# Kernel tuning notes

Hardware: AMD Instinct MI355X
Metric: run time of the kernel (lower is better)

The kernel has to match this reference:

```python
import jax, jax.numpy as jnp
import numpy as np

V, E, H, T = 100000, 128, 256, 7
B, S = 64, 512
START, STOP = 5, 6
H2 = H // 2


def setup_inputs() -> dict:
    key = jax.random.key(0)
    ks = jax.random.split(key, 16)
    rn = lambda k, shape, s=0.1: jax.random.normal(k, shape, jnp.float32) * s
    inp = {}
    inp["sentence"] = jax.random.randint(ks[0], (B, S), 0, V)
    inp["tags"] = jax.random.randint(ks[1], (B, S), 0, 5)
    inp["h0"] = jax.random.normal(ks[2], (2, B, H2), jnp.float32)
    inp["c0"] = jax.random.normal(ks[3], (2, B, H2), jnp.float32)
    inp["embedding"] = rn(ks[4], (V, E), 1.0)
    inp["w_ih_f"] = rn(ks[5], (4 * H2, E)); inp["w_hh_f"] = rn(ks[6], (4 * H2, H2))
    inp["b_ih_f"] = rn(ks[7], (4 * H2,)); inp["b_hh_f"] = rn(ks[8], (4 * H2,))
    inp["w_ih_b"] = rn(ks[9], (4 * H2, E)); inp["w_hh_b"] = rn(ks[10], (4 * H2, H2))
    inp["b_ih_b"] = rn(ks[11], (4 * H2,)); inp["b_hh_b"] = rn(ks[12], (4 * H2,))
    inp["w_out"] = rn(ks[13], (T, H)); inp["b_out"] = rn(ks[14], (T,))
    trans = jax.random.normal(ks[15], (T, T), jnp.float32)
    trans = trans.at[START, :].set(-10000.0).at[:, STOP].set(-10000.0)
    inp["transitions"] = trans
    return inp


def _lstm_dir(x, h0, c0, wih, whh, bih, bhh, reverse):
    # x: [S, B, E]; PyTorch gate order i, f, g, o
    def step(carry, xt):
        h, c = carry
        z = xt @ wih.T + h @ whh.T + bih + bhh  # [B, 4*H2]
        i, f, g, o = jnp.split(z, 4, axis=-1)
        c = jax.nn.sigmoid(f) * c + jax.nn.sigmoid(i) * jnp.tanh(g)
        h = jax.nn.sigmoid(o) * jnp.tanh(c)
        return (h, c), h
    _, hs = jax.lax.scan(step, (h0, c0), x, reverse=reverse)
    return hs  # [S, B, H2]


def reference(sentence, tags, h0, c0, embedding, w_ih_f, w_hh_f, b_ih_f, b_hh_f,
              w_ih_b, w_hh_b, b_ih_b, b_hh_b, w_out, b_out, transitions):
    # Embedding; torch code does .view(S, B, -1) on a [B, S, E] tensor (raw
    # reinterpretation) -- replicate with reshape to match the math exactly.
    embeds = embedding[sentence].reshape(S, B, E)
    hf = _lstm_dir(embeds, h0[0], c0[0], w_ih_f, w_hh_f, b_ih_f, b_hh_f, False)
    hb = _lstm_dir(embeds, h0[1], c0[1], w_ih_b, w_hh_b, b_ih_b, b_hh_b, True)
    feats = jnp.concatenate([hf, hb], axis=-1) @ w_out.T + b_out  # [S, B, T]

    # CRF forward algorithm. Original uses transitions.t(), i.e. step score
    # for prev=i -> next=j is transitions[i, j].
    alpha0 = jnp.full((B, T), -10000.0, jnp.float32).at[:, START].set(0.0)
    def crf_step(alpha, feat):
        # [b, i, j]: alpha[b,i] + transitions[i,j]; LSE over i, add emit[b,j]
        a = jax.nn.logsumexp(alpha[:, :, None] + transitions[None, :, :], axis=1) + feat
        return a, None
    alpha, _ = jax.lax.scan(crf_step, alpha0, feats)
    fwd_score = jax.nn.logsumexp(alpha + transitions[STOP][None, :], axis=1)  # [B]

    # Gold path score: transitions[next, prev] + emit[next], per _score_sentence.
    tags_ext = jnp.concatenate([jnp.full((B, 1), START, tags.dtype), tags], axis=1)
    t_prev, t_next = tags_ext[:, :-1], tags_ext[:, 1:]  # [B, S]
    trans_sc = transitions[t_next, t_prev].sum(axis=1)
    emit_sc = jnp.take_along_axis(jnp.transpose(feats, (1, 0, 2)),
                                  t_next[:, :, None], axis=2)[..., 0].sum(axis=1)
    gold = trans_sc + emit_sc + transitions[STOP, tags_ext[:, -1]]
    return jnp.sum(fwd_score - gold) / B
```

## Files before the change

kernel.cpp:

```cpp
#include <hip/hip_runtime.h>

typedef unsigned int u32;
typedef unsigned short u16;
typedef __attribute__((ext_vector_type(8))) short short8;
typedef __attribute__((ext_vector_type(4))) float f32x4;
typedef __attribute__((ext_vector_type(2))) float f32x2;

#define DEV __device__ __forceinline__
#define LOG2E 1.44269504089f

DEV u16 f2bf(float f) {
    u32 u = __float_as_uint(f);
    return (u16)((u + 0x7FFFu + ((u >> 16) & 1u)) >> 16);
}
DEV float bf2f(u16 h) { return __uint_as_float(((u32)h) << 16); }
DEV float frcp(float x) { return __builtin_amdgcn_rcpf(x); }
DEV float fexp2(float x) {
#if __has_builtin(__builtin_amdgcn_exp2f)
    return __builtin_amdgcn_exp2f(x);
#else
    return exp2f(x);
#endif
}
DEV u32 pack_bf16(float a, float b) {
#if __has_builtin(__builtin_amdgcn_cvt_pk_bf16_f32)
    auto v = __builtin_amdgcn_cvt_pk_bf16_f32(a, b);
    u32 r; __builtin_memcpy(&r, &v, 4); return r;
#else
    return (u32)f2bf(a) | ((u32)f2bf(b) << 16);
#endif
}
DEV float xex(uint2 v, int r) {
    u32 u = (r & 2) ? v.y : v.x;
    return (r & 1) ? __uint_as_float(u & 0xFFFF0000u) : __uint_as_float(u << 16);
}

DEV int gmap2(int g) { return ((g & 3) << 7) + (g & 0x7C) + (g >> 7); }

DEV f32x2 exp2p(f32x2 a) { f32x2 r; r.x = fexp2(a.x); r.y = fexp2(a.y); return r; }
DEV f32x2 rcpp(f32x2 a)  { f32x2 r; r.x = frcp(a.x);  r.y = frcp(a.y);  return r; }
DEV f32x2 minp(f32x2 a, float b) { f32x2 r; r.x = fminf(a.x, b); r.y = fminf(a.y, b); return r; }

DEV f32x2 lstm_pair(f32x2 zi, f32x2 zf, f32x2 zg, f32x2 zo, f32x2* cst) {
    f32x2 ei = exp2p(-zi);
    f32x2 ef = exp2p(-zf);
    f32x2 eo = exp2p(-zo);
    f32x2 eg = exp2p(minp(zg + zg, 115.f));
    f32x2 A = 1.f + ei, F = 1.f + ef, G = eg + 1.f, O = 1.f + eo;
    f32x2 AG = A * G;
    f32x2 cc = (*cst * AG + (eg - 1.f) * F) * rcpp(F * AG);
    *cst = cc;
    f32x2 ec = exp2p(minp(cc * 2.885390082f, 115.f));
    return (ec - 1.f) * rcpp(O * (ec + 1.f));
}

__global__ __launch_bounds__(512) void k_inproj2(
    const int* __restrict__ sent, const float* __restrict__ emb,
    const float* __restrict__ wihf, const float* __restrict__ bihf, const float* __restrict__ bhhf,
    const float* __restrict__ wihb, const float* __restrict__ bihb, const float* __restrict__ bhhb,
    u16* __restrict__ Xf, u16* __restrict__ Xb)
{
    int blk = blockIdx.x;
    int d  = blk >> 7;
    int sc = blk & 127;
    const float* wih = d ? wihb : wihf;
    const float* bih = d ? bihb : bihf;
    const float* bhh = d ? bhhb : bhhf;
    u16* X = d ? Xb : Xf;
    int tid = threadIdx.x;
    int w = tid >> 6, lane = tid & 63;
    int rg = lane >> 4, cn = lane & 15;

    short8 afr[4][4];
    #pragma unroll
    for (int mi = 0; mi < 4; ++mi) {
        int gate = gmap2(16 * (w + 8 * mi) + cn);
        #pragma unroll
        for (int kt = 0; kt < 4; ++kt) {
            const float* p = wih + (size_t)gate * 128 + kt * 32 + rg * 8;
            float4 f0 = *(const float4*)p;
            float4 f1 = *(const float4*)(p + 4);
            union { short8 v; u32 u[4]; } sv;
            sv.u[0] = pack_bf16(f0.x, f0.y);
            sv.u[1] = pack_bf16(f0.z, f0.w);
            sv.u[2] = pack_bf16(f1.x, f1.y);
            sv.u[3] = pack_bf16(f1.z, f1.w);
            afr[mi][kt] = sv.v;
        }
    }
    float bs[4][4];
    #pragma unroll
    for (int mi = 0; mi < 4; ++mi)
        #pragma unroll
        for (int r = 0; r < 4; ++r) {
            int g = gmap2(16 * (w + 8 * mi) + 4 * rg + r);
            bs[mi][r] = bih[g] + bhh[g];
        }

    __shared__ u16 tile[2][64][136];
    #pragma unroll
    for (int stage = 0; stage < 2; ++stage) {
        if (stage) __syncthreads();
        {
            int row = tid >> 2, q = tid & 3;
            int sl = row >> 6, bb = row & 63;
            int tok = sent[(sc * 4 + stage * 2 + sl) * 64 + bb];
            const float* er = emb + (size_t)tok * 128 + q * 32;
            u16* dst = &tile[sl][bb][q * 32];
            #pragma unroll
            for (int u = 0; u < 4; ++u) {
                float4 a = *(const float4*)(er + u * 8);
                float4 c = *(const float4*)(er + u * 8 + 4);
                uint4 st;
                st.x = pack_bf16(a.x, a.y); st.y = pack_bf16(a.z, a.w);
                st.z = pack_bf16(c.x, c.y); st.w = pack_bf16(c.z, c.w);
                *(uint4*)(dst + u * 8) = st;
            }
        }
        __syncthreads();
        #pragma unroll
        for (int ss = 0; ss < 2; ++ss) {
            int s = sc * 4 + stage * 2 + ss;
            #pragma unroll
            for (int nt = 0; nt < 4; ++nt) {
                short8 bfr[4];
                #pragma unroll
                for (int kt = 0; kt < 4; ++kt)
                    bfr[kt] = *(const short8*)&tile[ss][nt * 16 + cn][kt * 32 + rg * 8];
                #pragma unroll
                for (int mi = 0; mi < 4; ++mi) {
                    f32x4 acc = {0.f, 0.f, 0.f, 0.f};
                    #pragma unroll
                    for (int kt = 0; kt < 4; ++kt)
                        acc = __builtin_amdgcn_mfma_f32_16x16x32_bf16(afr[mi][kt], bfr[kt], acc, 0, 0, 0);
                    size_t base = (((size_t)s * 4 + nt) * 32 + (w + 8 * mi)) * 256
                                + (size_t)rg * 64 + (size_t)cn * 4;
                    uint2 st;
                    st.x = pack_bf16((acc[0] + bs[mi][0]) * LOG2E, (acc[1] + bs[mi][1]) * LOG2E);
                    st.y = pack_bf16((acc[2] + bs[mi][2]) * LOG2E, (acc[3] + bs[mi][3]) * LOG2E);
                    *(uint2*)(X + base) = st;
                }
            }
        }
    }
}

__global__ __launch_bounds__(512) void k_lstm(
    const float* __restrict__ h0, const float* __restrict__ c0,
    const float* __restrict__ whhf, const float* __restrict__ whhb,
    const u16* __restrict__ Xf, const u16* __restrict__ Xb,
    u16* __restrict__ hfo, u16* __restrict__ hbo)
{
    int d  = blockIdx.x >> 2, g4 = blockIdx.x & 3;
    const float* whh = d ? whhb : whhf;
    const u16*   X   = d ? Xb   : Xf;
    u16*         ho  = d ? hbo  : hfo;
    int w = threadIdx.x >> 6, lane = threadIdx.x & 63;
    int rg = lane >> 4, cn = lane & 15;

    short8 afr[4][4];
    #pragma unroll
    for (int mi = 0; mi < 4; ++mi) {
        int gate = gmap2(16 * (w + 8 * mi) + cn);
        #pragma unroll
        for (int kt = 0; kt < 4; ++kt) {
            const float* p = whh + (size_t)gate * 128 + kt * 32 + rg * 8;
            float4 f0 = *(const float4*)p;
            float4 f1 = *(const float4*)(p + 4);
            union { short8 v; u32 u[4]; } sv;
            sv.u[0] = pack_bf16(f0.x * LOG2E, f0.y * LOG2E);
            sv.u[1] = pack_bf16(f0.z * LOG2E, f0.w * LOG2E);
            sv.u[2] = pack_bf16(f1.x * LOG2E, f1.y * LOG2E);
            sv.u[3] = pack_bf16(f1.z * LOG2E, f1.w * LOG2E);
            afr[mi][kt] = sv.v;
        }
    }
    int b = g4 * 16 + cn;
    int chb = 16 * w + rg * 4;
    f32x2 cstA, cstB;
    {
        float4 cv = *(const float4*)(c0 + ((size_t)d * 64 + b) * 128 + chb);
        cstA.x = cv.x; cstA.y = cv.y;
        cstB.x = cv.z; cstB.y = cv.w;
    }
    __shared__ u16 hbuf[2][16][136];
    {
        float4 hv = *(const float4*)(h0 + ((size_t)d * 64 + b) * 128 + chb);
        uint2 st0;
        st0.x = pack_bf16(hv.x, hv.y);
        st0.y = pack_bf16(hv.z, hv.w);
        *(uint2*)&hbuf[0][cn][chb] = st0;
    }
    __syncthreads();

    int s0 = d ? 511 : 0;
    const int sdelta = d ? -32768 : 32768;
    const ptrdiff_t hdelta = d ? -8192 : 8192;
    size_t lof = (size_t)rg * 64 + (size_t)cn * 4;

    const u16* pa[4]; const u16* pb[4];
    uint2 xA[4], xB[4];
    #pragma unroll
    for (int mi = 0; mi < 4; ++mi) {
        const u16* base = X + (((size_t)s0 * 4 + g4) * 32 + (w + 8 * mi)) * 256 + lof;
        xA[mi] = *(const uint2*)base;
        xB[mi] = *(const uint2*)(base + sdelta);
        pa[mi] = base + 2 * sdelta;
        pb[mi] = base + 3 * sdelta;
    }
    u16* hop = ho + ((size_t)s0 * 64 + b) * 128 + chb;

#define LSTM_STEP(RB, WB, XC, XP)                                            \
    do {                                                                     \
        short8 bfr[4];                                                       \
        _Pragma("unroll")                                                    \
        for (int kt = 0; kt < 4; ++kt)                                       \
            bfr[kt] = *(const short8*)&hbuf[RB][cn][kt * 32 + rg * 8];       \
        f32x4 z[4];                                                          \
        _Pragma("unroll")                                                    \
        for (int mi = 0; mi < 4; ++mi) {                                     \
            f32x4 acc;                                                       \
            acc[0] = xex(XC[mi], 0); acc[1] = xex(XC[mi], 1);                \
            acc[2] = xex(XC[mi], 2); acc[3] = xex(XC[mi], 3);                \
            _Pragma("unroll")                                                \
            for (int kt = 0; kt < 4; ++kt)                                   \
                acc = __builtin_amdgcn_mfma_f32_16x16x32_bf16(               \
                    afr[mi][kt], bfr[kt], acc, 0, 0, 0);                     \
            z[mi] = acc;                                                     \
            XC[mi] = *(const uint2*)XP[mi];                                  \
            XP[mi] += 2 * sdelta;                                            \
        }                                                                    \
        f32x2 ziA = {z[0][0], z[1][0]}, zfA = {z[0][1], z[1][1]};            \
        f32x2 zgA = {z[0][2], z[1][2]}, zoA = {z[0][3], z[1][3]};            \
        f32x2 hA = lstm_pair(ziA, zfA, zgA, zoA, &cstA);                     \
        u32 pA = pack_bf16(hA.x, hA.y);                                      \
        *(u32*)&hbuf[WB][cn][chb] = pA;                                      \
        *(u32*)hop = pA;                                                     \
        f32x2 ziB = {z[2][0], z[3][0]}, zfB = {z[2][1], z[3][1]};            \
        f32x2 zgB = {z[2][2], z[3][2]}, zoB = {z[2][3], z[3][3]};            \
        f32x2 hB = lstm_pair(ziB, zfB, zgB, zoB, &cstB);                     \
        u32 pB = pack_bf16(hB.x, hB.y);                                      \
        *(u32*)&hbuf[WB][cn][chb + 2] = pB;                                  \
        *(u32*)(hop + 2) = pB;                                               \
        hop += hdelta;                                                       \
        asm volatile("s_waitcnt lgkmcnt(0)\n\ts_barrier" ::: "memory");      \
    } while (0)

    for (int it = 0; it < 256; ++it) {
        LSTM_STEP(0, 1, xA, pa);
        LSTM_STEP(1, 0, xB, pb);
    }
#undef LSTM_STEP
}

__global__ __launch_bounds__(256) void k_feats(
    const u16* __restrict__ hf, const u16* __restrict__ hb,
    const float* __restrict__ wout, const float* __restrict__ bout,
    float* __restrict__ feats)
{
    __shared__ u16 sf[32][136], sb[32][136];
    __shared__ float wo[7][260];
    __shared__ float bo[8];
    int tid = threadIdx.x;
    int pos0 = blockIdx.x * 32;
    {
        int r = tid >> 3, cc = (tid & 7) * 16;
        const uint4* pf = (const uint4*)(hf + (size_t)(pos0 + r) * 128 + cc);
        const uint4* pb = (const uint4*)(hb + (size_t)(pos0 + r) * 128 + cc);
        *(uint4*)&sf[r][cc]     = pf[0];
        *(uint4*)&sf[r][cc + 8] = pf[1];
        *(uint4*)&sb[r][cc]     = pb[0];
        *(uint4*)&sb[r][cc + 8] = pb[1];
    }
    for (int i = tid; i < 1792; i += 256) wo[i >> 8][i & 255] = wout[i];
    if (tid < 7) bo[tid] = bout[tid];
    __syncthreads();
    int pp = tid >> 3, tt = tid & 7;
    if (tt < 7) {
        float acc = bo[tt];
        #pragma unroll 4
        for (int ch = 0; ch < 128; ch += 2) {
            u32 uf = *(const u32*)&sf[pp][ch];
            u32 ub = *(const u32*)&sb[pp][ch];
            float2 w0 = *(const float2*)&wo[tt][ch];
            float2 w1 = *(const float2*)&wo[tt][128 + ch];
            acc += __uint_as_float(uf << 16) * w0.x
                 + __uint_as_float(uf & 0xFFFF0000u) * w0.y
                 + __uint_as_float(ub << 16) * w1.x
                 + __uint_as_float(ub & 0xFFFF0000u) * w1.y;
        }
        feats[(size_t)(pos0 + pp) * 7 + tt] = acc;
    }
}

__global__ __launch_bounds__(64) void k_crf_chunk(
    const float* __restrict__ feats, const float* __restrict__ trans,
    float* __restrict__ chunkM)
{
    int b = blockIdx.x >> 3, c = blockIdx.x & 7;
    int lane = threadIdx.x;
    int i = lane >> 3, j = lane & 7;
    __shared__ float fl[64][8];
    int s0 = c * 64;
    for (int idx = lane; idx < 448; idx += 64) {
        int ss = idx / 7, jj = idx - ss * 7;
        fl[ss][jj] = feats[(size_t)((s0 + ss) * 64 + b) * 7 + jj];
    }
    float tc[7];
    #pragma unroll
    for (int k = 0; k < 7; ++k) tc[k] = (j < 7) ? trans[k * 7 + j] : 0.f;
    bool valid = (i < 7 && j < 7);
    float M0 = valid ? trans[i * 7 + j] : -1e30f;
    __syncthreads();
    float M = M0 + (valid ? fl[0][j] : 0.f);
    for (int ss = 1; ss < 64; ++ss) {
        int rb = i * 8;
        float v0 = __shfl(M, rb + 0, 64) + tc[0];
        float v1 = __shfl(M, rb + 1, 64) + tc[1];
        float v2 = __shfl(M, rb + 2, 64) + tc[2];
        float v3 = __shfl(M, rb + 3, 64) + tc[3];
        float v4 = __shfl(M, rb + 4, 64) + tc[4];
        float v5 = __shfl(M, rb + 5, 64) + tc[5];
        float v6 = __shfl(M, rb + 6, 64) + tc[6];
        float mx = fmaxf(fmaxf(fmaxf(v0, v1), fmaxf(v2, v3)),
                         fmaxf(fmaxf(v4, v5), v6));
        float sm = __expf(v0 - mx) + __expf(v1 - mx) + __expf(v2 - mx)
                 + __expf(v3 - mx) + __expf(v4 - mx) + __expf(v5 - mx)
                 + __expf(v6 - mx);
        M = mx + __logf(sm) + fl[ss][j];
    }
    if (valid)
        chunkM[(size_t)(b * 8 + c) * 49 + i * 7 + j] = M;
}

__global__ __launch_bounds__(512) void k_crf_final(
    const float* __restrict__ chunkM, const float* __restrict__ trans,
    const int* __restrict__ tags, const float* __restrict__ feats,
    float* __restrict__ out)
{
    int tid = threadIdx.x;
    int w = tid >> 6, lane = tid & 63;
    int k = lane >> 3, j = lane & 7;
    int b = w * 8 + k;
    bool jv = (j < 7);
    __shared__ float Tl[49];
    __shared__ float red[512];
    __shared__ float fsh[64];
    if (tid < 49) Tl[tid] = trans[tid];
    __syncthreads();

    float av = (j == 5) ? 0.f : -1e4f;
    #pragma unroll
    for (int c = 0; c < 8; ++c) {
        float a0 = __shfl(av, k * 8 + 0, 64);
        float a1 = __shfl(av, k * 8 + 1, 64);
        float a2 = __shfl(av, k * 8 + 2, 64);
        float a3 = __shfl(av, k * 8 + 3, 64);
        float a4 = __shfl(av, k * 8 + 4, 64);
        float a5 = __shfl(av, k * 8 + 5, 64);
        float a6 = __shfl(av, k * 8 + 6, 64);
        if (jv) {
            const float* Pp = chunkM + ((size_t)b * 8 + c) * 49 + j;
            float v0 = a0 + Pp[0],  v1 = a1 + Pp[7],  v2 = a2 + Pp[14];
            float v3 = a3 + Pp[21], v4 = a4 + Pp[28], v5 = a5 + Pp[35];
            float v6 = a6 + Pp[42];
            float mx = fmaxf(fmaxf(fmaxf(v0, v1), fmaxf(v2, v3)),
                             fmaxf(fmaxf(v4, v5), v6));
            float sm = __expf(v0 - mx) + __expf(v1 - mx) + __expf(v2 - mx)
                     + __expf(v3 - mx) + __expf(v4 - mx) + __expf(v5 - mx)
                     + __expf(v6 - mx);
            av = mx + __logf(sm);
        }
    }
    float u = jv ? (av + Tl[42 + j]) : -1e30f;
    float m = u;
    #pragma unroll
    for (int off = 1; off < 8; off <<= 1) m = fmaxf(m, __shfl_xor(m, off, 64));
    float e = jv ? __expf(u - m) : 0.f;
    #pragma unroll
    for (int off = 1; off < 8; off <<= 1) e += __shfl_xor(e, off, 64);
    float fwd = m + __logf(e);
    if (j == 0) fsh[b] = fwd;

    int tb = tid & 63, q = tid >> 6;
    const int* tgp = tags + (size_t)tb * 512;
    float acc = 0.f;
    int tp = (q == 0) ? 5 : tgp[q * 64 - 1];
    for (int ss = q * 64; ss < q * 64 + 64; ++ss) {
        int tn = tgp[ss];
        acc += Tl[tn * 7 + tp] + feats[(size_t)(ss * 64 + tb) * 7 + tn];
        tp = tn;
    }
    if (q == 7) acc += Tl[42 + tgp[511]];
    red[tid] = acc;
    __syncthreads();
    if (tid < 64) {
        float g = red[tid];
        #pragma unroll
        for (int qq = 1; qq < 8; ++qq) g += red[tid + 64 * qq];
        red[tid] = fsh[tid] - g;
    }
    __syncthreads();
    if (tid < 64) {
        float v = red[tid];
        #pragma unroll
        for (int off = 1; off < 64; off <<= 1) v += __shfl_xor(v, off, 64);
        if (tid == 0) out[0] = v * (1.0f / 64.0f);
    }
}

extern "C" void kernel_launch(void* const* d_in, const int* in_sizes, int n_in,
                              void* d_out, int out_size, void* d_ws, size_t ws_size,
                              hipStream_t stream) {
    const int*   sent = (const int*)d_in[0];
    const int*   tags = (const int*)d_in[1];
    const float* h0   = (const float*)d_in[2];
    const float* c0   = (const float*)d_in[3];
    const float* emb  = (const float*)d_in[4];
    const float* wihf = (const float*)d_in[5];
    const float* whhf = (const float*)d_in[6];
    const float* bihf = (const float*)d_in[7];
    const float* bhhf = (const float*)d_in[8];
    const float* wihb = (const float*)d_in[9];
    const float* whhb = (const float*)d_in[10];
    const float* bihb = (const float*)d_in[11];
    const float* bhhb = (const float*)d_in[12];
    const float* wout = (const float*)d_in[13];
    const float* bout = (const float*)d_in[14];
    const float* trn  = (const float*)d_in[15];

    char* ws = (char*)d_ws;
    u16*   Xf     = (u16*)(ws);
    u16*   Xb     = (u16*)(ws + 33554432);
    u16*   hfp    = (u16*)(ws + 67108864);
    u16*   hbp    = (u16*)(ws + 75497472);
    float* feats  = (float*)(ws + 83886080);
    float* chunkM = (float*)(ws + 84803584);

    k_inproj2<<<256, 512, 0, stream>>>(sent, emb, wihf, bihf, bhhf,
                                       wihb, bihb, bhhb, Xf, Xb);
    k_lstm<<<8, 512, 0, stream>>>(h0, c0, whhf, whhb, Xf, Xb, hfp, hbp);
    k_feats<<<1024, 256, 0, stream>>>(hfp, hbp, wout, bout, feats);
    k_crf_chunk<<<512, 64, 0, stream>>>(feats, trn, chunkM);
    k_crf_final<<<1, 512, 0, stream>>>(chunkM, trn, tags, feats, (float*)d_out);
}
```

Baseline: 561.0 us.

## Split LSTM recurrence across 16 waves with new gate mapping

The recurrent LSTM kernel now launches 1024 threads (16 waves) per block instead of 512. Each wave handles two 16-row gate tiles instead of four, and each lane updates two hidden channels instead of four. A new gate permutation (gmap3) is applied consistently in both the input projection and the recurrence so that each lane's i/f/g/o values line up with the smaller tile split. The aim is to shorten the serial per-step critical path of MFMA and activation math. The cost is a larger per-step barrier across twice as many waves, plus more LDS traffic from reading h.

```diff
diff --git a/kernel.cpp b/kernel.cpp
--- a/kernel.cpp
+++ b/kernel.cpp
@@ -35,7 +35,9 @@
     return (r & 1) ? __uint_as_float(u & 0xFFFF0000u) : __uint_as_float(u << 16);
 }
 
-DEV int gmap2(int g) { return ((g & 3) << 7) + (g & 0x7C) + (g >> 7); }
+DEV int gmap3(int g) {
+    return ((g & 3) << 7) + ((g >> 5) << 3) + (((g >> 2) & 3) << 1) + ((g >> 4) & 1);
+}
 
 DEV f32x2 exp2p(f32x2 a) { f32x2 r; r.x = fexp2(a.x); r.y = fexp2(a.y); return r; }
 DEV f32x2 rcpp(f32x2 a)  { f32x2 r; r.x = frcp(a.x);  r.y = frcp(a.y);  return r; }
@@ -74,7 +76,7 @@
     short8 afr[4][4];
     #pragma unroll
     for (int mi = 0; mi < 4; ++mi) {
-        int gate = gmap2(16 * (w + 8 * mi) + cn);
+        int gate = gmap3(16 * (w + 8 * mi) + cn);
         #pragma unroll
         for (int kt = 0; kt < 4; ++kt) {
             const float* p = wih + (size_t)gate * 128 + kt * 32 + rg * 8;
@@ -93,7 +95,7 @@
     for (int mi = 0; mi < 4; ++mi)
         #pragma unroll
         for (int r = 0; r < 4; ++r) {
-            int g = gmap2(16 * (w + 8 * mi) + 4 * rg + r);
+            int g = gmap3(16 * (w + 8 * mi) + 4 * rg + r);
             bs[mi][r] = bih[g] + bhh[g];
         }
 
@@ -145,7 +147,7 @@
     }
 }
 
-__global__ __launch_bounds__(512) void k_lstm(
+__global__ __launch_bounds__(1024) void k_lstm(
     const float* __restrict__ h0, const float* __restrict__ c0,
     const float* __restrict__ whhf, const float* __restrict__ whhb,
     const u16* __restrict__ Xf, const u16* __restrict__ Xb,
@@ -158,10 +160,10 @@
     int w = threadIdx.x >> 6, lane = threadIdx.x & 63;
     int rg = lane >> 4, cn = lane & 15;
 
-    short8 afr[4][4];
-    #pragma unroll
-    for (int mi = 0; mi < 4; ++mi) {
-        int gate = gmap2(16 * (w + 8 * mi) + cn);
+    short8 afr[2][4];
+    #pragma unroll
+    for (int mi = 0; mi < 2; ++mi) {
+        int gate = gmap3(16 * (2 * w + mi) + cn);
         #pragma unroll
         for (int kt = 0; kt < 4; ++kt) {
             const float* p = whh + (size_t)gate * 128 + kt * 32 + rg * 8;
@@ -176,20 +178,16 @@
         }
     }
     int b = g4 * 16 + cn;
-    int chb = 16 * w + rg * 4;
-    f32x2 cstA, cstB;
+    int chq = 8 * w + 2 * rg;
+    f32x2 cst;
     {
-        float4 cv = *(const float4*)(c0 + ((size_t)d * 64 + b) * 128 + chb);
-        cstA.x = cv.x; cstA.y = cv.y;
-        cstB.x = cv.z; cstB.y = cv.w;
+        float2 cv = *(const float2*)(c0 + ((size_t)d * 64 + b) * 128 + chq);
+        cst.x = cv.x; cst.y = cv.y;
     }
     __shared__ u16 hbuf[2][16][136];
     {
-        float4 hv = *(const float4*)(h0 + ((size_t)d * 64 + b) * 128 + chb);
-        uint2 st0;
-        st0.x = pack_bf16(hv.x, hv.y);
-        st0.y = pack_bf16(hv.z, hv.w);
-        *(uint2*)&hbuf[0][cn][chb] = st0;
+        float2 hv = *(const float2*)(h0 + ((size_t)d * 64 + b) * 128 + chq);
+        *(u32*)&hbuf[0][cn][chq] = pack_bf16(hv.x, hv.y);
     }
     __syncthreads();
 
@@ -198,17 +196,17 @@
     const ptrdiff_t hdelta = d ? -8192 : 8192;
     size_t lof = (size_t)rg * 64 + (size_t)cn * 4;
 
-    const u16* pa[4]; const u16* pb[4];
-    uint2 xA[4], xB[4];
-    #pragma unroll
-    for (int mi = 0; mi < 4; ++mi) {
-        const u16* base = X + (((size_t)s0 * 4 + g4) * 32 + (w + 8 * mi)) * 256 + lof;
+    const u16* pa[2]; const u16* pb[2];
+    uint2 xA[2], xB[2];
+    #pragma unroll
+    for (int mi = 0; mi < 2; ++mi) {
+        const u16* base = X + (((size_t)s0 * 4 + g4) * 32 + (2 * w + mi)) * 256 + lof;
         xA[mi] = *(const uint2*)base;
         xB[mi] = *(const uint2*)(base + sdelta);
         pa[mi] = base + 2 * sdelta;
         pb[mi] = base + 3 * sdelta;
     }
-    u16* hop = ho + ((size_t)s0 * 64 + b) * 128 + chb;
+    u16* hop = ho + ((size_t)s0 * 64 + b) * 128 + chq;
 
 #define LSTM_STEP(RB, WB, XC, XP)                                            \
     do {                                                                     \
@@ -216,9 +214,9 @@
         _Pragma("unroll")                                                    \
         for (int kt = 0; kt < 4; ++kt)                                       \
             bfr[kt] = *(const short8*)&hbuf[RB][cn][kt * 32 + rg * 8];       \
-        f32x4 z[4];                                                          \
+        f32x4 z[2];                                                          \
         _Pragma("unroll")                                                    \
-        for (int mi = 0; mi < 4; ++mi) {                                     \
+        for (int mi = 0; mi < 2; ++mi) {                                     \
             f32x4 acc;                                                       \
             acc[0] = xex(XC[mi], 0); acc[1] = xex(XC[mi], 1);                \
             acc[2] = xex(XC[mi], 2); acc[3] = xex(XC[mi], 3);                \
@@ -230,18 +228,12 @@
             XC[mi] = *(const uint2*)XP[mi];                                  \
             XP[mi] += 2 * sdelta;                                            \
         }                                                                    \
-        f32x2 ziA = {z[0][0], z[1][0]}, zfA = {z[0][1], z[1][1]};            \
-        f32x2 zgA = {z[0][2], z[1][2]}, zoA = {z[0][3], z[1][3]};            \
-        f32x2 hA = lstm_pair(ziA, zfA, zgA, zoA, &cstA);                     \
-        u32 pA = pack_bf16(hA.x, hA.y);                                      \
-        *(u32*)&hbuf[WB][cn][chb] = pA;                                      \
-        *(u32*)hop = pA;                                                     \
-        f32x2 ziB = {z[2][0], z[3][0]}, zfB = {z[2][1], z[3][1]};            \
-        f32x2 zgB = {z[2][2], z[3][2]}, zoB = {z[2][3], z[3][3]};            \
-        f32x2 hB = lstm_pair(ziB, zfB, zgB, zoB, &cstB);                     \
-        u32 pB = pack_bf16(hB.x, hB.y);                                      \
-        *(u32*)&hbuf[WB][cn][chb + 2] = pB;                                  \
-        *(u32*)(hop + 2) = pB;                                               \
+        f32x2 zi = {z[0][0], z[1][0]}, zf = {z[0][1], z[1][1]};              \
+        f32x2 zg = {z[0][2], z[1][2]}, zo = {z[0][3], z[1][3]};              \
+        f32x2 h = lstm_pair(zi, zf, zg, zo, &cst);                           \
+        u32 p = pack_bf16(h.x, h.y);                                         \
+        *(u32*)&hbuf[WB][cn][chq] = p;                                       \
+        *(u32*)hop = p;                                                      \
         hop += hdelta;                                                       \
         asm volatile("s_waitcnt lgkmcnt(0)\n\ts_barrier" ::: "memory");      \
     } while (0)
@@ -439,7 +431,7 @@
 
     k_inproj2<<<256, 512, 0, stream>>>(sent, emb, wihf, bihf, bhhf,
                                        wihb, bihb, bhhb, Xf, Xb);
-    k_lstm<<<8, 512, 0, stream>>>(h0, c0, whhf, whhb, Xf, Xb, hfp, hbp);
+    k_lstm<<<8, 1024, 0, stream>>>(h0, c0, whhf, whhb, Xf, Xb, hfp, hbp);
     k_feats<<<1024, 256, 0, stream>>>(hfp, hbp, wout, bout, feats);
     k_crf_chunk<<<512, 64, 0, stream>>>(feats, trn, chunkM);
     k_crf_final<<<1, 512, 0, stream>>>(chunkM, trn, tags, feats, (float*)d_out);
```

After: 586.9 us. 1.05x slower.

## Fuse feats, CRF chunk, and CRF final into one tail kernel with ticket

Applied to the files above, without the earlier changes.

Merges the emission projection, per-chunk CRF matrix scan, gold-path scoring and final reduction into a single kernel. Each block computes its own feats in registers and shared memory instead of writing and re-reading a global feats buffer. The last block to finish, found with an atomic ticket counter reset by the LSTM kernel, does the cross-chunk combine. This removes two kernel launches and the feats round trip. In exchange, the final combine now runs on one 64-thread block serially over batch groups, and each thread loads a full 512-byte hidden row.

```diff
diff --git a/kernel.cpp b/kernel.cpp
--- a/kernel.cpp
+++ b/kernel.cpp
@@ -149,8 +149,9 @@
     const float* __restrict__ h0, const float* __restrict__ c0,
     const float* __restrict__ whhf, const float* __restrict__ whhb,
     const u16* __restrict__ Xf, const u16* __restrict__ Xb,
-    u16* __restrict__ hfo, u16* __restrict__ hbo)
+    u16* __restrict__ hfo, u16* __restrict__ hbo, u32* __restrict__ ctr)
 {
+    if (blockIdx.x == 0 && threadIdx.x == 0) *ctr = 0;
     int d  = blockIdx.x >> 2, g4 = blockIdx.x & 3;
     const float* whh = d ? whhb : whhf;
     const u16*   X   = d ? Xb   : Xf;
@@ -253,67 +254,67 @@
 #undef LSTM_STEP
 }
 
-__global__ __launch_bounds__(256) void k_feats(
+__global__ __launch_bounds__(64) void k_tail(
     const u16* __restrict__ hf, const u16* __restrict__ hb,
     const float* __restrict__ wout, const float* __restrict__ bout,
-    float* __restrict__ feats)
+    const float* __restrict__ trans, const int* __restrict__ tags,
+    float* __restrict__ chunkM, float* __restrict__ goldp,
+    u32* __restrict__ ctr, float* __restrict__ out)
 {
-    __shared__ u16 sf[32][136], sb[32][136];
+    int b = blockIdx.x >> 3, c = blockIdx.x & 7;
+    int ss = threadIdx.x;
+    int i = ss >> 3, j = ss & 7;
+    __shared__ float fl[64][8];
     __shared__ float wo[7][260];
+    __shared__ float Tl[49];
     __shared__ float bo[8];
-    int tid = threadIdx.x;
-    int pos0 = blockIdx.x * 32;
+    __shared__ float fsh[64];
+    for (int q = ss; q < 1792; q += 64) wo[q >> 8][q & 255] = wout[q];
+    if (ss < 49) Tl[ss] = trans[ss];
+    if (ss < 7) bo[ss] = bout[ss];
+    __syncthreads();
+
+    int s = c * 64 + ss;
+    union { uint4 v4[8]; u32 u[32]; } hfr, hbr;
     {
-        int r = tid >> 3, cc = (tid & 7) * 16;
-        const uint4* pf = (const uint4*)(hf + (size_t)(pos0 + r) * 128 + cc);
-        const uint4* pb = (const uint4*)(hb + (size_t)(pos0 + r) * 128 + cc);
-        *(uint4*)&sf[r][cc]     = pf[0];
-        *(uint4*)&sf[r][cc + 8] = pf[1];
-        *(uint4*)&sb[r][cc]     = pb[0];
-        *(uint4*)&sb[r][cc + 8] = pb[1];
-    }
-    for (int i = tid; i < 1792; i += 256) wo[i >> 8][i & 255] = wout[i];
-    if (tid < 7) bo[tid] = bout[tid];
-    __syncthreads();
-    int pp = tid >> 3, tt = tid & 7;
-    if (tt < 7) {
-        float acc = bo[tt];
-        #pragma unroll 4
-        for (int ch = 0; ch < 128; ch += 2) {
-            u32 uf = *(const u32*)&sf[pp][ch];
-            u32 ub = *(const u32*)&sb[pp][ch];
-            float2 w0 = *(const float2*)&wo[tt][ch];
-            float2 w1 = *(const float2*)&wo[tt][128 + ch];
+        const uint4* pf = (const uint4*)(hf + (size_t)(s * 64 + b) * 128);
+        const uint4* pb = (const uint4*)(hb + (size_t)(s * 64 + b) * 128);
+        #pragma unroll
+        for (int u2 = 0; u2 < 8; ++u2) { hfr.v4[u2] = pf[u2]; hbr.v4[u2] = pb[u2]; }
+    }
+    #pragma unroll
+    for (int t = 0; t < 7; ++t) {
+        float acc = bo[t];
+        #pragma unroll
+        for (int k = 0; k < 32; ++k) {
+            u32 uf = hfr.u[k];
+            u32 ub = hbr.u[k];
+            float2 w0 = *(const float2*)&wo[t][2 * k];
+            float2 w1 = *(const float2*)&wo[t][128 + 2 * k];
             acc += __uint_as_float(uf << 16) * w0.x
                  + __uint_as_float(uf & 0xFFFF0000u) * w0.y
                  + __uint_as_float(ub << 16) * w1.x
                  + __uint_as_float(ub & 0xFFFF0000u) * w1.y;
         }
-        feats[(size_t)(pos0 + pp) * 7 + tt] = acc;
-    }
-}
-
-__global__ __launch_bounds__(64) void k_crf_chunk(
-    const float* __restrict__ feats, const float* __restrict__ trans,
-    float* __restrict__ chunkM)
-{
-    int b = blockIdx.x >> 3, c = blockIdx.x & 7;
-    int lane = threadIdx.x;
-    int i = lane >> 3, j = lane & 7;
-    __shared__ float fl[64][8];
-    int s0 = c * 64;
-    for (int idx = lane; idx < 448; idx += 64) {
-        int ss = idx / 7, jj = idx - ss * 7;
-        fl[ss][jj] = feats[(size_t)((s0 + ss) * 64 + b) * 7 + jj];
-    }
+        fl[ss][t] = acc;
+    }
+    fl[ss][7] = 0.f;
+    __syncthreads();
+
+    int tn = tags[(size_t)b * 512 + s];
+    int tp = (s == 0) ? 5 : tags[(size_t)b * 512 + s - 1];
+    float gp = Tl[tn * 7 + tp] + fl[ss][tn];
+    if (c == 7 && ss == 63) gp += Tl[42 + tn];
+    #pragma unroll
+    for (int off = 1; off < 64; off <<= 1) gp += __shfl_xor(gp, off, 64);
+    if (ss == 0) goldp[b * 8 + c] = gp;
+
     float tc[7];
     #pragma unroll
-    for (int k = 0; k < 7; ++k) tc[k] = (j < 7) ? trans[k * 7 + j] : 0.f;
+    for (int k = 0; k < 7; ++k) tc[k] = (j < 7) ? Tl[k * 7 + j] : 0.f;
     bool valid = (i < 7 && j < 7);
-    float M0 = valid ? trans[i * 7 + j] : -1e30f;
-    __syncthreads();
-    float M = M0 + (valid ? fl[0][j] : 0.f);
-    for (int ss = 1; ss < 64; ++ss) {
+    float M = valid ? (Tl[i * 7 + j] + fl[0][j]) : -1e30f;
+    for (int s2 = 1; s2 < 64; ++s2) {
         int rb = i * 8;
         float v0 = __shfl(M, rb + 0, 64) + tc[0];
         float v1 = __shfl(M, rb + 1, 64) + tc[1];
@@ -327,86 +328,63 @@
         float sm = __expf(v0 - mx) + __expf(v1 - mx) + __expf(v2 - mx)
                  + __expf(v3 - mx) + __expf(v4 - mx) + __expf(v5 - mx)
                  + __expf(v6 - mx);
-        M = mx + __logf(sm) + fl[ss][j];
+        M = mx + __logf(sm) + fl[s2][j];
     }
     if (valid)
         chunkM[(size_t)(b * 8 + c) * 49 + i * 7 + j] = M;
-}
-
-__global__ __launch_bounds__(512) void k_crf_final(
-    const float* __restrict__ chunkM, const float* __restrict__ trans,
-    const int* __restrict__ tags, const float* __restrict__ feats,
-    float* __restrict__ out)
-{
-    int tid = threadIdx.x;
-    int w = tid >> 6, lane = tid & 63;
-    int k = lane >> 3, j = lane & 7;
-    int b = w * 8 + k;
+
+    __threadfence();
+    u32 ticket = 0;
+    if (ss == 0)
+        ticket = __hip_atomic_fetch_add(ctr, 1u, __ATOMIC_ACQ_REL,
+                                        __HIP_MEMORY_SCOPE_AGENT);
+    ticket = (u32)__shfl((int)ticket, 0, 64);
+    if (ticket != 511u) return;
+
     bool jv = (j < 7);
-    __shared__ float Tl[49];
-    __shared__ float red[512];
-    __shared__ float fsh[64];
-    if (tid < 49) Tl[tid] = trans[tid];
+    int k2 = i;
+    for (int wg = 0; wg < 8; ++wg) {
+        int b2 = wg * 8 + k2;
+        float av = (j == 5) ? 0.f : -1e4f;
+        #pragma unroll 1
+        for (int c2 = 0; c2 < 8; ++c2) {
+            float a0 = __shfl(av, k2 * 8 + 0, 64);
+            float a1 = __shfl(av, k2 * 8 + 1, 64);
+            float a2 = __shfl(av, k2 * 8 + 2, 64);
+            float a3 = __shfl(av, k2 * 8 + 3, 64);
+            float a4 = __shfl(av, k2 * 8 + 4, 64);
+            float a5 = __shfl(av, k2 * 8 + 5, 64);
+            float a6 = __shfl(av, k2 * 8 + 6, 64);
+            if (jv) {
+                const float* Pp = chunkM + ((size_t)b2 * 8 + c2) * 49 + j;
+                float v0 = a0 + Pp[0],  v1 = a1 + Pp[7],  v2 = a2 + Pp[14];
+                float v3 = a3 + Pp[21], v4 = a4 + Pp[28], v5 = a5 + Pp[35];
+                float v6 = a6 + Pp[42];
+                float mx = fmaxf(fmaxf(fmaxf(v0, v1), fmaxf(v2, v3)),
+                                 fmaxf(fmaxf(v4, v5), v6));
+                float sm = __expf(v0 - mx) + __expf(v1 - mx) + __expf(v2 - mx)
+                         + __expf(v3 - mx) + __expf(v4 - mx) + __expf(v5 - mx)
+                         + __expf(v6 - mx);
+                av = mx + __logf(sm);
+            }
+        }
+        float u2 = jv ? (av + Tl[42 + j]) : -1e30f;
+        float m = u2;
+        #pragma unroll
+        for (int off = 1; off < 8; off <<= 1) m = fmaxf(m, __shfl_xor(m, off, 64));
+        float e = jv ? __expf(u2 - m) : 0.f;
+        #pragma unroll
+        for (int off = 1; off < 8; off <<= 1) e += __shfl_xor(e, off, 64);
+        if (j == 0) fsh[b2] = m + __logf(e);
+    }
     __syncthreads();
-
-    float av = (j == 5) ? 0.f : -1e4f;
-    #pragma unroll
-    for (int c = 0; c < 8; ++c) {
-        float a0 = __shfl(av, k * 8 + 0, 64);
-        float a1 = __shfl(av, k * 8 + 1, 64);
-        float a2 = __shfl(av, k * 8 + 2, 64);
-        float a3 = __shfl(av, k * 8 + 3, 64);
-        float a4 = __shfl(av, k * 8 + 4, 64);
-        float a5 = __shfl(av, k * 8 + 5, 64);
-        float a6 = __shfl(av, k * 8 + 6, 64);
-        if (jv) {
-            const float* Pp = chunkM + ((size_t)b * 8 + c) * 49 + j;
-            float v0 = a0 + Pp[0],  v1 = a1 + Pp[7],  v2 = a2 + Pp[14];
-            float v3 = a3 + Pp[21], v4 = a4 + Pp[28], v5 = a5 + Pp[35];
-            float v6 = a6 + Pp[42];
-            float mx = fmaxf(fmaxf(fmaxf(v0, v1), fmaxf(v2, v3)),
-                             fmaxf(fmaxf(v4, v5), v6));
-            float sm = __expf(v0 - mx) + __expf(v1 - mx) + __expf(v2 - mx)
-                     + __expf(v3 - mx) + __expf(v4 - mx) + __expf(v5 - mx)
-                     + __expf(v6 - mx);
-            av = mx + __logf(sm);
-        }
-    }
-    float u = jv ? (av + Tl[42 + j]) : -1e30f;
-    float m = u;
-    #pragma unroll
-    for (int off = 1; off < 8; off <<= 1) m = fmaxf(m, __shfl_xor(m, off, 64));
-    float e = jv ? __expf(u - m) : 0.f;
-    #pragma unroll
-    for (int off = 1; off < 8; off <<= 1) e += __shfl_xor(e, off, 64);
-    float fwd = m + __logf(e);
-    if (j == 0) fsh[b] = fwd;
-
-    int tb = tid & 63, q = tid >> 6;
-    const int* tgp = tags + (size_t)tb * 512;
-    float acc = 0.f;
-    int tp = (q == 0) ? 5 : tgp[q * 64 - 1];
-    for (int ss = q * 64; ss < q * 64 + 64; ++ss) {
-        int tn = tgp[ss];
-        acc += Tl[tn * 7 + tp] + feats[(size_t)(ss * 64 + tb) * 7 + tn];
-        tp = tn;
-    }
-    if (q == 7) acc += Tl[42 + tgp[511]];
-    red[tid] = acc;
-    __syncthreads();
-    if (tid < 64) {
-        float g = red[tid];
-        #pragma unroll
-        for (int qq = 1; qq < 8; ++qq) g += red[tid + 64 * qq];
-        red[tid] = fsh[tid] - g;
-    }
-    __syncthreads();
-    if (tid < 64) {
-        float v = red[tid];
-        #pragma unroll
-        for (int off = 1; off < 64; off <<= 1) v += __shfl_xor(v, off, 64);
-        if (tid == 0) out[0] = v * (1.0f / 64.0f);
-    }
+    float g = 0.f;
+    #pragma unroll
+    for (int c3 = 0; c3 < 8; ++c3) g += goldp[ss * 8 + c3];
+    float v = fsh[ss] - g;
+    #pragma unroll
+    for (int off = 1; off < 64; off <<= 1) v += __shfl_xor(v, off, 64);
+    if (ss == 0) out[0] = v * (1.0f / 64.0f);
 }
 
 extern "C" void kernel_launch(void* const* d_in, const int* in_sizes, int n_in,
@@ -434,13 +412,13 @@
     u16*   Xb     = (u16*)(ws + 33554432);
     u16*   hfp    = (u16*)(ws + 67108864);
     u16*   hbp    = (u16*)(ws + 75497472);
-    float* feats  = (float*)(ws + 83886080);
+    float* goldp  = (float*)(ws + 83886080);
+    u32*   ctr    = (u32*)(ws + 83888128);
     float* chunkM = (float*)(ws + 84803584);
 
     k_inproj2<<<256, 512, 0, stream>>>(sent, emb, wihf, bihf, bhhf,
                                        wihb, bihb, bhhb, Xf, Xb);
-    k_lstm<<<8, 512, 0, stream>>>(h0, c0, whhf, whhb, Xf, Xb, hfp, hbp);
-    k_feats<<<1024, 256, 0, stream>>>(hfp, hbp, wout, bout, feats);
-    k_crf_chunk<<<512, 64, 0, stream>>>(feats, trn, chunkM);
-    k_crf_final<<<1, 512, 0, stream>>>(chunkM, trn, tags, feats, (float*)d_out);
-}
+    k_lstm<<<8, 512, 0, stream>>>(h0, c0, whhf, whhb, Xf, Xb, hfp, hbp, ctr);
+    k_tail<<<512, 64, 0, stream>>>(hfp, hbp, wout, bout, trn, tags,
+                                   chunkM, goldp, ctr, (float*)d_out);
+}
```

After: 584.8 us. 1.04x slower.
